# Kernel tuning notes

Measured on AMD Instinct MI355X. Metric: run time of the kernel, lower is better.

## Reference

```python
import jax, jax.numpy as jnp
import numpy as np

# Model dims (match init_kwargs)
B, L, D = 1, 2048, 1024
DI = 2048          # D_inner
N = 16             # SSM state size
DR = 64            # delta_rank
K = 4              # conv_1d_size
EPS = 1e-5
DELTA_MIN, DELTA_MAX, DELTA_FLOOR = 1e-3, 1e-1, 1e-4


def setup_inputs() -> dict:
    key = jax.random.key(0)
    ks = jax.random.split(key, 9)
    g = lambda i, shape, scale: (jax.random.normal(ks[i], shape, jnp.float32) * scale)
    x = g(0, (B, L, D), 1.0)
    rms_w = jnp.ones((D,), jnp.float32)
    in_proj_w = g(1, (D, 2 * DI), D ** -0.5)           # Linear D -> 2*DI, no bias
    conv_w = g(2, (DI, K), 0.3)                         # depthwise conv kernel
    conv_b = g(3, (DI,), 0.1)
    bcd_w = g(4, (DI, 2 * N + DR), DI ** -0.5)          # to_BCdelta, no bias
    dup_w = g(5, (DR, DI), DR ** -0.5)                  # delta_upscale weight
    # delta_upscale bias: inverse-softplus of log-uniform samples in [delta_min, delta_max]
    u = jax.random.uniform(ks[6], (DI,), jnp.float32)
    samples = jnp.clip(jnp.exp(u * (np.log(DELTA_MAX) - np.log(DELTA_MIN)) + np.log(DELTA_MIN)), DELTA_FLOOR)
    dup_b = samples + jnp.log(-jnp.expm1(-samples))
    # log(-A) with A = -[1..N] repeated over channels (S4D-real init)
    log_minus_A = jnp.tile(jnp.log(jnp.arange(1, N + 1, dtype=jnp.float32))[None, :], (DI, 1))
    D_param = jnp.ones((DI,), jnp.float32)              # skip parameter D
    out_proj_w = g(7, (DI, D), DI ** -0.5)              # Linear DI -> D, no bias
    return {"x": x, "rms_w": rms_w, "in_proj_w": in_proj_w, "conv_w": conv_w,
            "conv_b": conv_b, "bcd_w": bcd_w, "dup_w": dup_w, "dup_b": dup_b,
            "log_minus_A": log_minus_A, "D_param": D_param, "out_proj_w": out_proj_w}


def reference(x, rms_w, in_proj_w, conv_w, conv_b, bcd_w, dup_w, dup_b,
              log_minus_A, D_param, out_proj_w):
    b, l, _ = x.shape
    # RMSNorm
    xn = x * jax.lax.rsqrt(jnp.mean(x * x, axis=-1, keepdims=True) + EPS) * rms_w
    # in_proj and split into ssm branch / gating residual branch
    proj = xn @ in_proj_w                                  # (b,l,2*DI)
    xs, res = proj[..., :DI], proj[..., DI:]
    # causal depthwise conv1d (torch pads K-1 both sides then truncates -> left-pad only)
    xp = jnp.pad(xs, ((0, 0), (K - 1, 0), (0, 0)))         # (b,l+K-1,DI)
    conv = sum(xp[:, k:k + l, :] * conv_w[:, k] for k in range(K)) + conv_b
    xc = jax.nn.silu(conv)                                 # (b,l,DI)
    # S6 block
    bcd = xc @ bcd_w                                       # (b,l,DR+2N)
    delta_lr = bcd[..., :DR]
    Bm = bcd[..., DR:DR + N]                               # (b,l,N)
    Cm = bcd[..., DR + N:]                                 # (b,l,N)
    delta = jax.nn.softplus(delta_lr @ dup_w + dup_b)      # (b,l,DI)
    A = -jnp.exp(log_minus_A)                              # (DI,N)
    A_bar = jnp.exp(jnp.einsum('bld,dn->bldn', delta, A))  # (b,l,DI,N)
    B_bar_x = jnp.einsum('bld,bln,bld->bldn', delta, Bm, xc)
    # sequential selective scan: h_t = A_bar_t * h_{t-1} + B_bar_x_t
    def step(h, ab_bx):
        ab, bx = ab_bx
        h = ab * h + bx
        return h, h
    h0 = jnp.zeros((b, DI, N), x.dtype)
    _, hs = jax.lax.scan(step, h0, (jnp.swapaxes(A_bar, 0, 1), jnp.swapaxes(B_bar_x, 0, 1)))
    # hs: (l,b,DI,N); project out with C and add skip D
    y = jnp.einsum('bln,lbdn->bld', Cm, hs) + xc * D_param
    # gate, out_proj, residual
    y = y * jax.nn.silu(res)
    return y @ out_proj_w + x
```

## Files before the change

kernel.cpp:

```cpp
#include <hip/hip_runtime.h>
#include <hip/hip_bf16.h>
#include <math.h>

#define Lseq 2048
#define Dmod 1024
#define DI   2048
#define Nst  16
#define DRr  64
#define NCHUNK 32
#define LCHUNK 64
#define SPLITK 16
#define OSPLIT 4

typedef unsigned short u16;
typedef float  f32x4  __attribute__((ext_vector_type(4)));
typedef short  short8 __attribute__((ext_vector_type(8)));

__device__ __forceinline__ float sigmoidf_(float x) { return 1.f / (1.f + expf(-x)); }
__device__ __forceinline__ float softplusf_(float x) {
    return fmaxf(x, 0.f) + log1pf(expf(-fabsf(x)));
}
__device__ __forceinline__ u16 f2bf(float x) {
    union { float f; unsigned u; } v; v.f = x;
    unsigned r = (v.u + 0x7fffu + ((v.u >> 16) & 1u)) >> 16;
    return (u16)r;
}
__device__ __forceinline__ float bf2f(u16 h) {
    union { unsigned u; float f; } v; v.u = ((unsigned)h) << 16; return v.f;
}
__device__ __forceinline__ void async16(const void* g, void* l) {
    __builtin_amdgcn_global_load_lds((__attribute__((address_space(1))) void*)g,
                                     (__attribute__((address_space(3))) void*)l, 16, 0, 0);
}

struct __align__(8) u16x4 { u16 x, y, z, w; };

__global__ __launch_bounds__(256) void rmsnorm_split_k(const float* __restrict__ x,
                                                       const float* __restrict__ w,
                                                       u16* __restrict__ xh,
                                                       u16* __restrict__ xl) {
    int row = blockIdx.x;
    int tid = threadIdx.x;
    float4 v = reinterpret_cast<const float4*>(x + (size_t)row * Dmod)[tid];
    float ss = v.x * v.x + v.y * v.y + v.z * v.z + v.w * v.w;
    #pragma unroll
    for (int m = 32; m >= 1; m >>= 1) ss += __shfl_xor(ss, m);
    __shared__ float s4[4];
    if ((tid & 63) == 0) s4[tid >> 6] = ss;
    __syncthreads();
    float tot = s4[0] + s4[1] + s4[2] + s4[3];
    float scale = rsqrtf(tot * (1.0f / Dmod) + 1e-5f);
    float4 wv = reinterpret_cast<const float4*>(w)[tid];
    float o[4] = {v.x * scale * wv.x, v.y * scale * wv.y,
                  v.z * scale * wv.z, v.w * scale * wv.w};
    u16x4 H, L;
    u16* hp = &H.x; u16* lp = &L.x;
    #pragma unroll
    for (int q = 0; q < 4; q++) {
        u16 h = f2bf(o[q]); hp[q] = h; lp[q] = f2bf(o[q] - bf2f(h));
    }
    reinterpret_cast<u16x4*>(xh + (size_t)row * Dmod)[tid] = H;
    reinterpret_cast<u16x4*>(xl + (size_t)row * Dmod)[tid] = L;
}

__device__ __forceinline__ void wsplit_body(const float* __restrict__ W, int R, int Cn,
                                            int bx, int by, float (*t)[33],
                                            u16* __restrict__ Th, u16* __restrict__ Tl) {
    int r0 = by * 32, c0 = bx * 32;
    int tr = threadIdx.x >> 3;
    int tc4 = (threadIdx.x & 7) * 4;
    float4 v = *reinterpret_cast<const float4*>(&W[(size_t)(r0 + tr) * Cn + c0 + tc4]);
    t[tr][tc4 + 0] = v.x; t[tr][tc4 + 1] = v.y;
    t[tr][tc4 + 2] = v.z; t[tr][tc4 + 3] = v.w;
    __syncthreads();
    u16x4 H, L;
    u16* hp = &H.x; u16* lp = &L.x;
    #pragma unroll
    for (int q = 0; q < 4; q++) {
        float xv = t[tc4 + q][tr];
        u16 h = f2bf(xv); hp[q] = h; lp[q] = f2bf(xv - bf2f(h));
    }
    size_t o = (size_t)(c0 + tr) * R + r0 + tc4;
    *reinterpret_cast<u16x4*>(&Th[o]) = H;
    *reinterpret_cast<u16x4*>(&Tl[o]) = L;
}

__global__ __launch_bounds__(256) void wsplitT_k(const float* __restrict__ W, int R, int Cn,
                                                 u16* __restrict__ Th, u16* __restrict__ Tl) {
    __shared__ float t[32][33];
    wsplit_body(W, R, Cn, blockIdx.x, blockIdx.y, t, Th, Tl);
}

__global__ __launch_bounds__(256) void wsplit3_k(const float* __restrict__ Wo,
                                                 const float* __restrict__ Wb,
                                                 const float* __restrict__ Wd,
                                                 u16* WoH, u16* WoL,
                                                 u16* bwTH, u16* bwTL,
                                                 u16* dwTH, u16* dwTL) {
    __shared__ float t[32][33];
    int b = blockIdx.x;
    if (b < 2048) {
        wsplit_body(Wo, 2048, 1024, b & 31, b >> 5, t, WoH, WoL);
    } else if (b < 2240) {
        int bb = b - 2048;
        wsplit_body(Wb, 2048, 96, bb % 3, bb / 3, t, bwTH, bwTL);
    } else {
        int bb = b - 2240;
        wsplit_body(Wd, 64, 2048, bb & 63, bb >> 6, t, dwTH, dwTL);
    }
}

template <int BM, int BN, int EPI>
__global__ __launch_bounds__(256) void gemm_mfma3(
    const u16* __restrict__ Ah, const u16* __restrict__ Al,
    const u16* __restrict__ Bh, const u16* __restrict__ Bl,
    float* __restrict__ C, float* __restrict__ C2, const float* __restrict__ aux,
    int M, int N, int K) {
    constexpr int BK = 32;
    constexpr int MF = BM / 32, NF = BN / 32;
    constexpr int CH_A = BM / 16, CH_B = BN / 16;
    __shared__ u16 AhT[2][BM][BK], AlT[2][BM][BK], BhT[2][BN][BK], BlT[2][BN][BK];
    const int tid = threadIdx.x, lane = tid & 63, wid = tid >> 6;
    const int wr = wid >> 1, wc = wid & 1;
    const int lr = lane & 15;
    const int sw = (lane >> 1) & 3;
    const int lkq = ((lane >> 4) ^ sw) * 8;
    const int bm0 = blockIdx.y * BM, bn0 = blockIdx.x * BN;
    const int srow = lane >> 2;
    const int scol_ = ((lane & 3) ^ ((lane >> 3) & 3)) * 8;

    int kbeg = 0, kend = K;
    if (EPI == 5) {
        int ks = K / gridDim.z;
        kbeg = blockIdx.z * ks;
        kend = kbeg + ks;
    }
    const int nt = (kend - kbeg) / BK;

    auto STAGE = [&](int buf, int k0) {
        int ci = 0;
        #pragma unroll
        for (int c = 0; c < CH_A; c++, ci++) if ((ci & 3) == wid) {
            size_t g = (size_t)(bm0 + c * 16 + srow) * K + (k0 + scol_);
            async16(Ah + g, (u16*)&AhT[buf][0][0] + c * 512 + lane * 8);
        }
        #pragma unroll
        for (int c = 0; c < CH_A; c++, ci++) if ((ci & 3) == wid) {
            size_t g = (size_t)(bm0 + c * 16 + srow) * K + (k0 + scol_);
            async16(Al + g, (u16*)&AlT[buf][0][0] + c * 512 + lane * 8);
        }
        #pragma unroll
        for (int c = 0; c < CH_B; c++, ci++) if ((ci & 3) == wid) {
            size_t g = (size_t)(bn0 + c * 16 + srow) * K + (k0 + scol_);
            async16(Bh + g, (u16*)&BhT[buf][0][0] + c * 512 + lane * 8);
        }
        #pragma unroll
        for (int c = 0; c < CH_B; c++, ci++) if ((ci & 3) == wid) {
            size_t g = (size_t)(bn0 + c * 16 + srow) * K + (k0 + scol_);
            async16(Bl + g, (u16*)&BlT[buf][0][0] + c * 512 + lane * 8);
        }
    };

    f32x4 acc[MF][NF];
    #pragma unroll
    for (int i = 0; i < MF; i++)
        #pragma unroll
        for (int j = 0; j < NF; j++) acc[i][j] = (f32x4){0.f, 0.f, 0.f, 0.f};

    STAGE(0, kbeg);
    asm volatile("s_waitcnt vmcnt(0)" ::: "memory");
    __builtin_amdgcn_s_barrier();

    for (int t = 0; t < nt; ++t) {
        const int cur = t & 1;
        if (t + 1 < nt) STAGE(cur ^ 1, kbeg + (t + 1) * BK);

        short8 ah[MF], al[MF], bh[NF], bl[NF];
        #pragma unroll
        for (int i = 0; i < MF; i++) {
            int r = wr * (MF * 16) + i * 16 + lr;
            ah[i] = *(const short8*)&AhT[cur][r][lkq];
            al[i] = *(const short8*)&AlT[cur][r][lkq];
        }
        #pragma unroll
        for (int j = 0; j < NF; j++) {
            int r = wc * (NF * 16) + j * 16 + lr;
            bh[j] = *(const short8*)&BhT[cur][r][lkq];
            bl[j] = *(const short8*)&BlT[cur][r][lkq];
        }
        asm volatile("s_waitcnt lgkmcnt(0)" ::: "memory");
        __builtin_amdgcn_sched_barrier(0);
        __builtin_amdgcn_s_setprio(1);
        #pragma unroll
        for (int i = 0; i < MF; i++)
            #pragma unroll
            for (int j = 0; j < NF; j++) {
                acc[i][j] = __builtin_amdgcn_mfma_f32_16x16x32_bf16(ah[i], bh[j], acc[i][j], 0, 0, 0);
                acc[i][j] = __builtin_amdgcn_mfma_f32_16x16x32_bf16(ah[i], bl[j], acc[i][j], 0, 0, 0);
                acc[i][j] = __builtin_amdgcn_mfma_f32_16x16x32_bf16(al[i], bh[j], acc[i][j], 0, 0, 0);
            }
        __builtin_amdgcn_s_setprio(0);
        if (t + 1 < nt) {
            asm volatile("s_waitcnt vmcnt(0)" ::: "memory");
            __builtin_amdgcn_s_barrier();
        }
    }

    float* Cp = C;
    if (EPI == 5) Cp = C + (size_t)blockIdx.z * M * N;
    #pragma unroll
    for (int i = 0; i < MF; i++)
        #pragma unroll
        for (int j = 0; j < NF; j++) {
            int rowg = bm0 + wr * (MF * 16) + i * 16 + (lane >> 4) * 4;
            int colg = bn0 + wc * (NF * 16) + j * 16 + lr;
            #pragma unroll
            for (int q = 0; q < 4; q++) {
                float v = acc[i][j][q];
                if (EPI == 5) {
                    Cp[(size_t)(rowg + q) * N + colg] = v;
                } else if (EPI == 2) {
                    C[(size_t)(rowg + q) * N + colg] = softplusf_(v + aux[colg]);
                } else if (EPI == 4) {
                    if (colg < DI) C[(size_t)(rowg + q) * DI + colg] = v;
                    else C2[(size_t)(rowg + q) * DI + (colg - DI)] = v * sigmoidf_(v);
                }
            }
        }
}

__global__ __launch_bounds__(256) void bcd_reduce_k(const float* __restrict__ partial,
                                                    float* __restrict__ bcd,
                                                    u16* __restrict__ bH,
                                                    u16* __restrict__ bL) {
    const int NT = Lseq * 96;
    int t = blockIdx.x * 256 + threadIdx.x;
    float s = 0.f;
    #pragma unroll
    for (int z = 0; z < SPLITK; z++) s += partial[(size_t)z * NT + t];
    bcd[t] = s;
    int col = t % 96, row = t / 96;
    if (col < DRr) {
        u16 h = f2bf(s);
        bH[(size_t)row * DRr + col] = h;
        bL[(size_t)row * DRr + col] = f2bf(s - bf2f(h));
    }
}

__global__ __launch_bounds__(256) void out_reduce_k(const float* __restrict__ part,
                                                    const float* __restrict__ x,
                                                    float* __restrict__ out) {
    int t = blockIdx.x * 256 + threadIdx.x;
    const size_t NT = (size_t)Lseq * Dmod;
    float4 xv = reinterpret_cast<const float4*>(x)[t];
    float4 o = xv;
    #pragma unroll
    for (int z = 0; z < OSPLIT; z++) {
        float4 p = reinterpret_cast<const float4*>(part + (size_t)z * NT)[t];
        o.x += p.x; o.y += p.y; o.z += p.z; o.w += p.w;
    }
    reinterpret_cast<float4*>(out)[t] = o;
}

__global__ __launch_bounds__(256) void conv_silu_k(const float* __restrict__ xs,
                                                   const float* __restrict__ cw,
                                                   const float* __restrict__ cb,
                                                   u16* __restrict__ xcH,
                                                   u16* __restrict__ xcL) {
    int d = blockIdx.x * 256 + threadIdx.x;
    int l = blockIdx.y;
    float4 w = reinterpret_cast<const float4*>(cw)[d];
    float wk[4] = {w.x, w.y, w.z, w.w};
    float s = cb[d];
    #pragma unroll
    for (int k = 0; k < 4; k++) {
        int ls = l - 3 + k;
        if (ls >= 0) s = fmaf(xs[(size_t)ls * DI + d], wk[k], s);
    }
    float v = s * sigmoidf_(s);
    size_t o = (size_t)l * DI + d;
    u16 h = f2bf(v);
    xcH[o] = h;
    xcL[o] = f2bf(v - bf2f(h));
}

__global__ __launch_bounds__(256) void scan1_k(const float* __restrict__ delta,
                                               const u16* __restrict__ xcH,
                                               const u16* __restrict__ xcL,
                                               const float* __restrict__ bcd,
                                               const float* __restrict__ lmA,
                                               float* __restrict__ Pb,
                                               float* __restrict__ Sb) {
    __shared__ float Bs[LCHUNK][16];
    const int tid = threadIdx.x;
    const int d = (blockIdx.x * 256 + tid) >> 1;
    const int half = tid & 1;
    const int c = blockIdx.y;
    const int l0 = c * LCHUNK;
    {
        int row = tid >> 2, q = (tid & 3) * 4;
        float4 v = *reinterpret_cast<const float4*>(&bcd[(size_t)(l0 + row) * 96 + DRr + q]);
        *reinterpret_cast<float4*>(&Bs[row][q]) = v;
    }
    __syncthreads();
    float negA[8], h[8];
    #pragma unroll
    for (int j = 0; j < 8; j++) {
        negA[j] = -__expf(lmA[(size_t)d * Nst + half * 8 + j]);
        h[j] = 0.f;
    }
    float sdv = 0.f;
    for (int l = 0; l < LCHUNK; ++l) {
        size_t o = (size_t)(l0 + l) * DI + d;
        float dv = delta[o];
        float xcv = bf2f(xcH[o]) + bf2f(xcL[o]);
        sdv += dv;
        float dvx = dv * xcv;
        #pragma unroll
        for (int j = 0; j < 8; j++) {
            float a = __expf(dv * negA[j]);
            h[j] = fmaf(a, h[j], dvx * Bs[l][half * 8 + j]);
        }
    }
    size_t base = ((size_t)c * DI + d) * Nst + half * 8;
    #pragma unroll
    for (int j = 0; j < 8; j++) {
        Pb[base + j] = __expf(sdv * negA[j]);
        Sb[base + j] = h[j];
    }
}

__global__ __launch_bounds__(256) void scan2_k(float* __restrict__ PH,
                                               const float* __restrict__ Sb) {
    int t = blockIdx.x * 256 + threadIdx.x;
    float H = 0.f;
    for (int c = 0; c < NCHUNK; c++) {
        size_t idx = (size_t)c * (DI * Nst) + t;
        float P = PH[idx], S = Sb[idx];
        PH[idx] = H;
        H = S + P * H;
    }
}

__global__ __launch_bounds__(256) void scan3_k(const float* __restrict__ delta,
                                               const u16* __restrict__ xcH,
                                               const u16* __restrict__ xcL,
                                               const float* __restrict__ bcd,
                                               const float* __restrict__ lmA,
                                               const float* __restrict__ Dp,
                                               const float* __restrict__ gate,
                                               const float* __restrict__ Hinit,
                                               u16* __restrict__ yH,
                                               u16* __restrict__ yL) {
    __shared__ float BCs[LCHUNK][32];
    const int tid = threadIdx.x;
    const int d = (blockIdx.x * 256 + tid) >> 1;
    const int half = tid & 1;
    const int c = blockIdx.y;
    const int l0 = c * LCHUNK;
    #pragma unroll
    for (int i = 0; i < 2; i++) {
        int idx = tid + 256 * i;
        int row = idx >> 3, q = (idx & 7) * 4;
        float4 v = *reinterpret_cast<const float4*>(&bcd[(size_t)(l0 + row) * 96 + DRr + q]);
        *reinterpret_cast<float4*>(&BCs[row][q]) = v;
    }
    __syncthreads();
    float negA[8], h[8];
    size_t hbase = ((size_t)c * DI + d) * Nst + half * 8;
    #pragma unroll
    for (int j = 0; j < 8; j++) {
        negA[j] = -__expf(lmA[(size_t)d * Nst + half * 8 + j]);
        h[j] = Hinit[hbase + j];
    }
    float Dpv = Dp[d];
    for (int l = 0; l < LCHUNK; ++l) {
        size_t o = (size_t)(l0 + l) * DI + d;
        float dv = delta[o];
        float xcv = bf2f(xcH[o]) + bf2f(xcL[o]);
        float dvx = dv * xcv;
        float yp = 0.f;
        #pragma unroll
        for (int j = 0; j < 8; j++) {
            float a = __expf(dv * negA[j]);
            h[j] = fmaf(a, h[j], dvx * BCs[l][half * 8 + j]);
            yp = fmaf(BCs[l][16 + half * 8 + j], h[j], yp);
        }
        yp += __shfl_xor(yp, 1);
        if (half == 0) {
            float yv = (yp + xcv * Dpv) * gate[o];
            u16 hq = f2bf(yv);
            yH[o] = hq;
            yL[o] = f2bf(yv - bf2f(hq));
        }
    }
}

extern "C" void kernel_launch(void* const* d_in, const int* in_sizes, int n_in,
                              void* d_out, int out_size, void* d_ws, size_t ws_size,
                              hipStream_t stream) {
    const float* x          = (const float*)d_in[0];
    const float* rms_w      = (const float*)d_in[1];
    const float* in_proj_w  = (const float*)d_in[2];
    const float* conv_w     = (const float*)d_in[3];
    const float* conv_b     = (const float*)d_in[4];
    const float* bcd_w      = (const float*)d_in[5];
    const float* dup_w      = (const float*)d_in[6];
    const float* dup_b      = (const float*)d_in[7];
    const float* lmA        = (const float*)d_in[8];
    const float* Dp         = (const float*)d_in[9];
    const float* out_proj_w = (const float*)d_in[10];
    float* out = (float*)d_out;
    char*  W   = (char*)d_ws;

    const size_t MB = 1ull << 20;
    u16*   WiH  = (u16*)(W + 0);
    u16*   WiL  = (u16*)(W + 8 * MB);
    float* delta= (float*)(W + 0);
    float* xs   = (float*)(W + 16 * MB);
    float* part = (float*)(W + 16 * MB);
    u16*   bwTH = (u16*)(W + 28 * MB);
    u16*   bwTL = (u16*)(W + 28 * MB + 384 * 1024);
    u16*   dwTH = (u16*)(W + 28 * MB + 768 * 1024);
    u16*   dwTL = (u16*)(W + 28 * MB + 1024 * 1024);
    u16*   bcdH = (u16*)(W + 28 * MB + 1280 * 1024);
    u16*   bcdL = (u16*)(W + 28 * MB + 1536 * 1024);
    float* Sb   = (float*)(W + 16 * MB);
    u16*   yH   = (u16*)(W + 16 * MB);
    u16*   yL   = (u16*)(W + 24 * MB);
    float* gate = (float*)(W + 32 * MB);
    u16*   xcH  = (u16*)(W + 48 * MB);
    u16*   xcL  = (u16*)(W + 56 * MB);
    float* opart= (float*)(W + 32 * MB);
    u16*   xnH  = (u16*)(W + 64 * MB);
    u16*   xnL  = (u16*)(W + 68 * MB);
    u16*   WoH  = (u16*)(W + 64 * MB);
    u16*   WoL  = (u16*)(W + 68 * MB);
    float* bcd  = (float*)(W + 72 * MB);
    float* Pb   = (float*)(W + 73 * MB);

    rmsnorm_split_k<<<Lseq, 256, 0, stream>>>(x, rms_w, xnH, xnL);
    wsplitT_k<<<dim3(4096 / 32, 1024 / 32), 256, 0, stream>>>(in_proj_w, 1024, 4096, WiH, WiL);
    gemm_mfma3<128, 128, 4><<<dim3(4096 / 128, Lseq / 128), 256, 0, stream>>>(
        xnH, xnL, WiH, WiL, xs, gate, nullptr, Lseq, 2 * DI, Dmod);
    conv_silu_k<<<dim3(DI / 256, Lseq), 256, 0, stream>>>(xs, conv_w, conv_b, xcH, xcL);
    wsplit3_k<<<2368, 256, 0, stream>>>(out_proj_w, bcd_w, dup_w,
                                        WoH, WoL, bwTH, bwTL, dwTH, dwTL);
    gemm_mfma3<128, 96, 5><<<dim3(1, Lseq / 128, SPLITK), 256, 0, stream>>>(
        xcH, xcL, bwTH, bwTL, part, nullptr, nullptr, Lseq, 96, DI);
    bcd_reduce_k<<<Lseq * 96 / 256, 256, 0, stream>>>(part, bcd, bcdH, bcdL);
    gemm_mfma3<64, 128, 2><<<dim3(DI / 128, Lseq / 64), 256, 0, stream>>>(
        bcdH, bcdL, dwTH, dwTL, delta, nullptr, dup_b, Lseq, DI, DRr);
    scan1_k<<<dim3(16, NCHUNK), 256, 0, stream>>>(delta, xcH, xcL, bcd, lmA, Pb, Sb);
    scan2_k<<<dim3(DI * Nst / 256), 256, 0, stream>>>(Pb, Sb);
    scan3_k<<<dim3(16, NCHUNK), 256, 0, stream>>>(delta, xcH, xcL, bcd, lmA, Dp, gate, Pb, yH, yL);
    gemm_mfma3<128, 128, 5><<<dim3(Dmod / 128, Lseq / 128, OSPLIT), 256, 0, stream>>>(
        yH, yL, WoH, WoL, opart, nullptr, nullptr, Lseq, Dmod, DI);
    out_reduce_k<<<Lseq * Dmod / 1024, 256, 0, stream>>>(opart, x, out);
}
```

Baseline: 245.6 us.

## Deepen GEMM prefetch, fuse rmsnorm with weight split, and tile conv over sequence

The GEMM mainloop now issues loads two K-tiles ahead. It waits with a partial vmcnt instead of draining all loads each iteration, so global-to-LDS copies overlap with MFMA work. The rmsnorm and in_proj weight-split kernels are merged into one launch, which saves a kernel launch. The conv+SiLU kernel now walks 32 sequence positions per thread with a sliding register window, so each input is read once instead of four times. The partial-wait counts are hand-coded per tile shape and rely on the load count per thread matching NLD, which is fragile if that count differs.

```diff
diff --git a/kernel.cpp b/kernel.cpp
--- a/kernel.cpp
+++ b/kernel.cpp
@@ -32,36 +32,14 @@
     __builtin_amdgcn_global_load_lds((__attribute__((address_space(1))) void*)g,
                                      (__attribute__((address_space(3))) void*)l, 16, 0, 0);
 }
+template <int N> __device__ __forceinline__ void vmwait() {
+    if constexpr (N == 0)      asm volatile("s_waitcnt vmcnt(0)" ::: "memory");
+    else if constexpr (N == 6) asm volatile("s_waitcnt vmcnt(6)" ::: "memory");
+    else if constexpr (N == 7) asm volatile("s_waitcnt vmcnt(7)" ::: "memory");
+    else                       asm volatile("s_waitcnt vmcnt(8)" ::: "memory");
+}
 
 struct __align__(8) u16x4 { u16 x, y, z, w; };
-
-__global__ __launch_bounds__(256) void rmsnorm_split_k(const float* __restrict__ x,
-                                                       const float* __restrict__ w,
-                                                       u16* __restrict__ xh,
-                                                       u16* __restrict__ xl) {
-    int row = blockIdx.x;
-    int tid = threadIdx.x;
-    float4 v = reinterpret_cast<const float4*>(x + (size_t)row * Dmod)[tid];
-    float ss = v.x * v.x + v.y * v.y + v.z * v.z + v.w * v.w;
-    #pragma unroll
-    for (int m = 32; m >= 1; m >>= 1) ss += __shfl_xor(ss, m);
-    __shared__ float s4[4];
-    if ((tid & 63) == 0) s4[tid >> 6] = ss;
-    __syncthreads();
-    float tot = s4[0] + s4[1] + s4[2] + s4[3];
-    float scale = rsqrtf(tot * (1.0f / Dmod) + 1e-5f);
-    float4 wv = reinterpret_cast<const float4*>(w)[tid];
-    float o[4] = {v.x * scale * wv.x, v.y * scale * wv.y,
-                  v.z * scale * wv.z, v.w * scale * wv.w};
-    u16x4 H, L;
-    u16* hp = &H.x; u16* lp = &L.x;
-    #pragma unroll
-    for (int q = 0; q < 4; q++) {
-        u16 h = f2bf(o[q]); hp[q] = h; lp[q] = f2bf(o[q] - bf2f(h));
-    }
-    reinterpret_cast<u16x4*>(xh + (size_t)row * Dmod)[tid] = H;
-    reinterpret_cast<u16x4*>(xl + (size_t)row * Dmod)[tid] = L;
-}
 
 __device__ __forceinline__ void wsplit_body(const float* __restrict__ W, int R, int Cn,
                                             int bx, int by, float (*t)[33],
@@ -85,10 +63,39 @@
     *reinterpret_cast<u16x4*>(&Tl[o]) = L;
 }
 
-__global__ __launch_bounds__(256) void wsplitT_k(const float* __restrict__ W, int R, int Cn,
-                                                 u16* __restrict__ Th, u16* __restrict__ Tl) {
+__global__ __launch_bounds__(256) void prep1_k(const float* __restrict__ x,
+                                               const float* __restrict__ rms_w,
+                                               u16* __restrict__ xnH, u16* __restrict__ xnL,
+                                               const float* __restrict__ Wi,
+                                               u16* __restrict__ WiH, u16* __restrict__ WiL) {
     __shared__ float t[32][33];
-    wsplit_body(W, R, Cn, blockIdx.x, blockIdx.y, t, Th, Tl);
+    __shared__ float s4[4];
+    int b = blockIdx.x;
+    if (b < 2048) {
+        int row = b, tid = threadIdx.x;
+        float4 v = reinterpret_cast<const float4*>(x + (size_t)row * Dmod)[tid];
+        float ss = v.x * v.x + v.y * v.y + v.z * v.z + v.w * v.w;
+        #pragma unroll
+        for (int m = 32; m >= 1; m >>= 1) ss += __shfl_xor(ss, m);
+        if ((tid & 63) == 0) s4[tid >> 6] = ss;
+        __syncthreads();
+        float tot = s4[0] + s4[1] + s4[2] + s4[3];
+        float scale = rsqrtf(tot * (1.0f / Dmod) + 1e-5f);
+        float4 wv = reinterpret_cast<const float4*>(rms_w)[tid];
+        float o[4] = {v.x * scale * wv.x, v.y * scale * wv.y,
+                      v.z * scale * wv.z, v.w * scale * wv.w};
+        u16x4 H, L;
+        u16* hp = &H.x; u16* lp = &L.x;
+        #pragma unroll
+        for (int q = 0; q < 4; q++) {
+            u16 h = f2bf(o[q]); hp[q] = h; lp[q] = f2bf(o[q] - bf2f(h));
+        }
+        reinterpret_cast<u16x4*>(xnH + (size_t)row * Dmod)[tid] = H;
+        reinterpret_cast<u16x4*>(xnL + (size_t)row * Dmod)[tid] = L;
+    } else {
+        int bb = b - 2048;
+        wsplit_body(Wi, 1024, 4096, bb & 127, bb >> 7, t, WiH, WiL);
+    }
 }
 
 __global__ __launch_bounds__(256) void wsplit3_k(const float* __restrict__ Wo,
@@ -119,6 +126,7 @@
     constexpr int BK = 32;
     constexpr int MF = BM / 32, NF = BN / 32;
     constexpr int CH_A = BM / 16, CH_B = BN / 16;
+    constexpr int NLD = (2 * CH_A + 2 * CH_B) / 4;
     __shared__ u16 AhT[2][BM][BK], AlT[2][BM][BK], BhT[2][BN][BK], BlT[2][BN][BK];
     const int tid = threadIdx.x, lane = tid & 63, wid = tid >> 6;
     const int wr = wid >> 1, wc = wid & 1;
@@ -168,12 +176,12 @@
         for (int j = 0; j < NF; j++) acc[i][j] = (f32x4){0.f, 0.f, 0.f, 0.f};
 
     STAGE(0, kbeg);
-    asm volatile("s_waitcnt vmcnt(0)" ::: "memory");
-    __builtin_amdgcn_s_barrier();
+    if (nt > 1) STAGE(1, kbeg + BK);
 
     for (int t = 0; t < nt; ++t) {
         const int cur = t & 1;
-        if (t + 1 < nt) STAGE(cur ^ 1, kbeg + (t + 1) * BK);
+        if (t < nt - 1) vmwait<NLD>(); else vmwait<0>();
+        __builtin_amdgcn_s_barrier();
 
         short8 ah[MF], al[MF], bh[NF], bl[NF];
         #pragma unroll
@@ -190,6 +198,9 @@
         }
         asm volatile("s_waitcnt lgkmcnt(0)" ::: "memory");
         __builtin_amdgcn_sched_barrier(0);
+        __builtin_amdgcn_s_barrier();
+        if (t + 2 < nt) STAGE(cur, kbeg + (t + 2) * BK);
+
         __builtin_amdgcn_s_setprio(1);
         #pragma unroll
         for (int i = 0; i < MF; i++)
@@ -200,10 +211,6 @@
                 acc[i][j] = __builtin_amdgcn_mfma_f32_16x16x32_bf16(al[i], bh[j], acc[i][j], 0, 0, 0);
             }
         __builtin_amdgcn_s_setprio(0);
-        if (t + 1 < nt) {
-            asm volatile("s_waitcnt vmcnt(0)" ::: "memory");
-            __builtin_amdgcn_s_barrier();
-        }
     }
 
     float* Cp = C;
@@ -268,20 +275,29 @@
                                                    u16* __restrict__ xcH,
                                                    u16* __restrict__ xcL) {
     int d = blockIdx.x * 256 + threadIdx.x;
-    int l = blockIdx.y;
+    int l0 = blockIdx.y * 32;
     float4 w = reinterpret_cast<const float4*>(cw)[d];
-    float wk[4] = {w.x, w.y, w.z, w.w};
-    float s = cb[d];
-    #pragma unroll
-    for (int k = 0; k < 4; k++) {
-        int ls = l - 3 + k;
-        if (ls >= 0) s = fmaf(xs[(size_t)ls * DI + d], wk[k], s);
-    }
-    float v = s * sigmoidf_(s);
-    size_t o = (size_t)l * DI + d;
-    u16 h = f2bf(v);
-    xcH[o] = h;
-    xcL[o] = f2bf(v - bf2f(h));
+    float b = cb[d];
+    float p0 = 0.f, p1 = 0.f, p2 = 0.f;
+    if (l0 > 0) {
+        p0 = xs[(size_t)(l0 - 3) * DI + d];
+        p1 = xs[(size_t)(l0 - 2) * DI + d];
+        p2 = xs[(size_t)(l0 - 1) * DI + d];
+    }
+    for (int l = l0; l < l0 + 32; ++l) {
+        float c = xs[(size_t)l * DI + d];
+        float s = b;
+        s = fmaf(p0, w.x, s);
+        s = fmaf(p1, w.y, s);
+        s = fmaf(p2, w.z, s);
+        s = fmaf(c,  w.w, s);
+        float v = s * sigmoidf_(s);
+        size_t o = (size_t)l * DI + d;
+        u16 h = f2bf(v);
+        xcH[o] = h;
+        xcL[o] = f2bf(v - bf2f(h));
+        p0 = p1; p1 = p2; p2 = c;
+    }
 }
 
 __global__ __launch_bounds__(256) void scan1_k(const float* __restrict__ delta,
@@ -439,11 +455,10 @@
     float* bcd  = (float*)(W + 72 * MB);
     float* Pb   = (float*)(W + 73 * MB);
 
-    rmsnorm_split_k<<<Lseq, 256, 0, stream>>>(x, rms_w, xnH, xnL);
-    wsplitT_k<<<dim3(4096 / 32, 1024 / 32), 256, 0, stream>>>(in_proj_w, 1024, 4096, WiH, WiL);
+    prep1_k<<<2048 + 4096, 256, 0, stream>>>(x, rms_w, xnH, xnL, in_proj_w, WiH, WiL);
     gemm_mfma3<128, 128, 4><<<dim3(4096 / 128, Lseq / 128), 256, 0, stream>>>(
         xnH, xnL, WiH, WiL, xs, gate, nullptr, Lseq, 2 * DI, Dmod);
-    conv_silu_k<<<dim3(DI / 256, Lseq), 256, 0, stream>>>(xs, conv_w, conv_b, xcH, xcL);
+    conv_silu_k<<<dim3(DI / 256, Lseq / 32), 256, 0, stream>>>(xs, conv_w, conv_b, xcH, xcL);
     wsplit3_k<<<2368, 256, 0, stream>>>(out_proj_w, bcd_w, dup_w,
                                         WoH, WoL, bwTH, bwTL, dwTH, dwTL);
     gemm_mfma3<128, 96, 5><<<dim3(1, Lseq / 128, SPLITK), 256, 0, stream>>>(
```

Result: faster. 238.2 us (-3.0%).
